# Optimization experiments

Hardware: AMD Instinct MI355X
Metric: run time of the kernel (lower is better)

Reference implementation:

```python
import jax, jax.numpy as jnp
import numpy as np

B, S, D, H = 8, 2048, 1024, 1024

def setup_inputs() -> dict:
    key = jax.random.key(0)
    ks = jax.random.split(key, 7)
    s = 1.0 / np.sqrt(D)  # torch Linear default init scale (uniform bound)
    x = jax.random.normal(ks[0], (B, S, D), dtype=jnp.float32)
    Wq = jax.random.uniform(ks[1], (D, H), jnp.float32, -s, s)
    bq = jax.random.uniform(ks[2], (H,), jnp.float32, -s, s)
    Wk = jax.random.uniform(ks[3], (D, H), jnp.float32, -s, s)
    bk = jax.random.uniform(ks[4], (H,), jnp.float32, -s, s)
    Wv = jax.random.uniform(ks[5], (D, H), jnp.float32, -s, s)
    bv = jax.random.uniform(ks[6], (H,), jnp.float32, -s, s)
    return {"x": x, "Wq": Wq, "bq": bq, "Wk": Wk, "bk": bk, "Wv": Wv, "bv": bv}

def reference(x, Wq, bq, Wk, bk, Wv, bv):
    scale = jnp.asarray(H ** 0.5, x.dtype)
    q = jnp.einsum('bsd,dh->bsh', x, Wq) + bq
    k = jnp.einsum('bsd,dh->bsh', x, Wk) + bk
    v = jnp.einsum('bsd,dh->bsh', x, Wv) + bv
    scores = jnp.einsum('bqh,bkh->bqk', q, k) / scale  # [B,S,S]
    probs = jax.nn.softmax(scores, axis=-1)
    return jnp.einsum('bqk,bkh->bqh', probs, v)
```

## Files before the change

kernel.cpp:

```cpp
#include <hip/hip_runtime.h>
#include <hip/hip_bf16.h>
#include <stdint.h>

using bf16 = __hip_bfloat16;
typedef __bf16 bf16x8 __attribute__((ext_vector_type(8)));
typedef float f32x4 __attribute__((ext_vector_type(4)));
typedef unsigned short u16x8 __attribute__((ext_vector_type(8)));

#define GLOAD_LDS16(gp, lp)                                                    \
  __builtin_amdgcn_global_load_lds(                                           \
      (const __attribute__((address_space(1))) void*)(gp),                     \
      (__attribute__((address_space(3))) void*)(lp), 16, 0, 0)

#define WAITCNT_VM(N) asm volatile("s_waitcnt vmcnt(" #N ")" ::: "memory")
#define SB0() __builtin_amdgcn_sched_barrier(0)

__device__ inline void store_out(bf16* p, float v)  { *p = __float2bfloat16(v); }
__device__ inline void store_out(float* p, float v) { *p = v; }

template <typename OUT_T, int BIAS_AXIS, bool NFAST>
__global__ __launch_bounds__(256, 2) void gemm_bm(
    const bf16* __restrict__ A, const bf16* __restrict__ Bt,
    const float* __restrict__ bias0, const float* __restrict__ bias1,
    OUT_T* __restrict__ out0, OUT_T* __restrict__ out1, int Nsplit,
    int K, int lda, int ldb, int ldc,
    long long sA, long long sB, long long sC, float alpha)
{
    __shared__ __align__(16) bf16 lds[36864];

    const int Mt = gridDim.x, Nt = gridDim.y;
    const int nwg = Mt * Nt * gridDim.z;
    const int hw  = blockIdx.x + Mt * (blockIdx.y + Nt * blockIdx.z);
    const int lg  = (nwg & 7) ? hw : ((hw & 7) * (nwg >> 3) + (hw >> 3));
    const int per = Mt * Nt;
    const int zt  = lg / per;
    const int rem = lg - zt * per;
    int mt, nt;
    if (NFAST) { mt = rem / Nt; nt = rem - mt * Nt; }
    else       { mt = rem % Mt; nt = rem / Mt; }

    A  += (long long)zt * sA;
    Bt += (long long)zt * sB;
    out0 += (long long)zt * sC;
    if (out1) out1 += (long long)zt * sC;

    const int bm = mt * 256;
    const int bn = nt * 128;
    const int t = threadIdx.x, lane = t & 63, w = t >> 6;
    const int wm = w >> 1, wn = w & 1;
    const int fr = lane & 15, c16 = lane >> 4;

    const bf16* gA[4];
    const bf16* gB[2];
    #pragma unroll
    for (int k = 0; k < 4; ++k) {
        const int idx = t + 256 * k, r = idx >> 2, c = idx & 3;
        gA[k] = A + (long long)(bm + r) * lda + ((c ^ ((r >> 1) & 3)) << 3);
    }
    #pragma unroll
    for (int k = 0; k < 2; ++k) {
        const int idx = t + 256 * k, r = idx >> 2, c = idx & 3;
        gB[k] = Bt + (long long)(bn + r) * ldb + ((c ^ ((r >> 1) & 3)) << 3);
    }
    const int dstA = t * 8;
    const int dstB = 8192 + t * 8;

#define STAGE(JT, SLOTB) do {                                                  \
    GLOAD_LDS16(gA[0] + (JT) * 32, &lds[(SLOTB) + dstA]);                      \
    GLOAD_LDS16(gA[1] + (JT) * 32, &lds[(SLOTB) + dstA + 2048]);               \
    GLOAD_LDS16(gA[2] + (JT) * 32, &lds[(SLOTB) + dstA + 4096]);               \
    GLOAD_LDS16(gA[3] + (JT) * 32, &lds[(SLOTB) + dstA + 6144]);               \
    GLOAD_LDS16(gB[0] + (JT) * 32, &lds[(SLOTB) + dstB]);                      \
    GLOAD_LDS16(gB[1] + (JT) * 32, &lds[(SLOTB) + dstB + 2048]);               \
} while (0)

    const int swz8 = (c16 ^ ((fr >> 1) & 3)) << 3;
    const int offA = (wm * 128 + fr) * 32 + swz8;
    const int offB = 8192 + (wn * 64 + fr) * 32 + swz8;

    const int nk = K >> 5;

    STAGE(0, 0); STAGE(1, 12288);
    WAITCNT_VM(6);
    __builtin_amdgcn_s_barrier();

    f32x4 acc[8][4] = {};

    int slotb = 0;
    for (int j = 0; j < nk; ++j) {
        SB0();

        bf16x8 af[8], bfv[4];
        #pragma unroll
        for (int m = 0; m < 8; ++m)
            af[m] = *reinterpret_cast<const bf16x8*>(&lds[slotb + offA + m * 512]);
        #pragma unroll
        for (int n = 0; n < 4; ++n)
            bfv[n] = *reinterpret_cast<const bf16x8*>(&lds[slotb + offB + n * 512]);

        if (j + 2 < nk) {
            int s2 = slotb + 24576; if (s2 >= 36864) s2 -= 36864;
            STAGE(j + 2, s2);
        }

        #pragma unroll
        for (int m = 0; m < 8; ++m)
            #pragma unroll
            for (int n = 0; n < 4; ++n)
                acc[m][n] = __builtin_amdgcn_mfma_f32_16x16x32_bf16(
                    af[m], bfv[n], acc[m][n], 0, 0, 0);

        SB0();
        if (j + 2 < nk)      { WAITCNT_VM(6); }
        else if (j + 1 < nk) { WAITCNT_VM(0); }
        __builtin_amdgcn_s_barrier();

        slotb += 12288; if (slotb == 36864) slotb = 0;
    }

    const int colbase = bn + wn * 64 + fr;
    const int rowbase = bm + wm * 128 + c16 * 4;
    #pragma unroll
    for (int n = 0; n < 4; ++n) {
        const int gc = colbase + n * 16;
        const bool seg0 = gc < Nsplit;
        OUT_T* op = seg0 ? out0 : out1;
        const int col = seg0 ? gc : gc - Nsplit;
        float bcol = 0.0f;
        if (BIAS_AXIS == 0) {
            const float* bp = seg0 ? bias0 : bias1;
            if (bp) bcol = bp[col];
        }
        #pragma unroll
        for (int m = 0; m < 8; ++m) {
            #pragma unroll
            for (int jj = 0; jj < 4; ++jj) {
                const int row = rowbase + m * 16 + jj;
                float v = acc[m][n][jj] * alpha;
                if (BIAS_AXIS == 0) v += bcol;
                else if (bias0)     v += bias0[row];
                store_out(&op[(long long)row * ldc + col], v);
            }
        }
    }
#undef STAGE
}

__global__ __launch_bounds__(256) void f32_to_bf16(
    const float* __restrict__ in, bf16* __restrict__ out, long long n)
{
    long long i = ((long long)blockIdx.x * 256 + threadIdx.x) * 4;
    const long long stride = (long long)gridDim.x * 256 * 4;
    for (; i < n; i += stride) {
        float4 v = *reinterpret_cast<const float4*>(in + i);
        unsigned ux = __float_as_uint(v.x), uy = __float_as_uint(v.y);
        unsigned uz = __float_as_uint(v.z), uw = __float_as_uint(v.w);
        ushort4 o;
        o.x = (unsigned short)((ux + 0x7fffu + ((ux >> 16) & 1u)) >> 16);
        o.y = (unsigned short)((uy + 0x7fffu + ((uy >> 16) & 1u)) >> 16);
        o.z = (unsigned short)((uz + 0x7fffu + ((uz >> 16) & 1u)) >> 16);
        o.w = (unsigned short)((uw + 0x7fffu + ((uw >> 16) & 1u)) >> 16);
        *reinterpret_cast<ushort4*>(out + i) = o;
    }
}

__global__ void transpose_f32_bf16(const float* __restrict__ in,
                                   bf16* __restrict__ out, int R, int C)
{
    __shared__ float tile[32][33];
    const int c0 = blockIdx.x * 32, r0 = blockIdx.y * 32;
    const int tx = threadIdx.x, ty = threadIdx.y;
    #pragma unroll
    for (int i = ty; i < 32; i += 8)
        tile[i][tx] = in[(long long)(r0 + i) * C + (c0 + tx)];
    __syncthreads();
    #pragma unroll
    for (int i = ty; i < 32; i += 8)
        out[(long long)(c0 + i) * R + (r0 + tx)] = __float2bfloat16(tile[tx][i]);
}

__global__ __launch_bounds__(256) void softmax_rows(bf16* __restrict__ Sbuf, int cols)
{
    __shared__ float red[8];
    bf16* p = Sbuf + (long long)blockIdx.x * cols;
    const int t = threadIdx.x;

    u16x8 v = *reinterpret_cast<const u16x8*>(p + t * 8);
    float f[8];
    #pragma unroll
    for (int i = 0; i < 8; ++i)
        f[i] = __uint_as_float((unsigned)v[i] << 16);

    float m = -3.0e38f;
    #pragma unroll
    for (int i = 0; i < 8; ++i) m = fmaxf(m, f[i]);
    #pragma unroll
    for (int o = 32; o; o >>= 1) m = fmaxf(m, __shfl_xor(m, o));
    if ((t & 63) == 0) red[t >> 6] = m;
    __syncthreads();
    m = fmaxf(fmaxf(red[0], red[1]), fmaxf(red[2], red[3]));

    float s = 0.0f;
    #pragma unroll
    for (int i = 0; i < 8; ++i) { f[i] = __expf(f[i] - m); s += f[i]; }
    #pragma unroll
    for (int o = 32; o; o >>= 1) s += __shfl_xor(s, o);
    __syncthreads();
    if ((t & 63) == 0) red[4 + (t >> 6)] = s;
    __syncthreads();
    s = (red[4] + red[5]) + (red[6] + red[7]);
    const float inv = 1.0f / s;

    u16x8 o16;
    #pragma unroll
    for (int i = 0; i < 8; ++i) {
        unsigned u = __float_as_uint(f[i] * inv);
        o16[i] = (unsigned short)((u + 0x7fffu + ((u >> 16) & 1u)) >> 16);
    }
    *reinterpret_cast<u16x8*>(p + t * 8) = o16;
}

extern "C" void kernel_launch(void* const* d_in, const int* in_sizes, int n_in,
                              void* d_out, int out_size, void* d_ws, size_t ws_size,
                              hipStream_t stream)
{
    const int B = 8, S = 2048, D = 1024, H = 1024;
    const float* x  = (const float*)d_in[0];
    const float* Wq = (const float*)d_in[1];
    const float* bq = (const float*)d_in[2];
    const float* Wk = (const float*)d_in[3];
    const float* bk = (const float*)d_in[4];
    const float* Wv = (const float*)d_in[5];
    const float* bv = (const float*)d_in[6];
    float* out = (float*)d_out;

    const size_t nQKV = (size_t)B * S * H;
    const size_t nW   = (size_t)D * H;
    const long long sSH = (long long)S * H;
    const long long sSS = (long long)S * S;

    dim3 tb(32, 8), g256(256);
    const float inv_scale = 1.0f / 32.0f;

    bf16* xb   = (bf16*)d_ws;
    bf16* Q    = xb  + nQKV;
    bf16* Kb   = Q   + nQKV;
    bf16* Vt   = Kb  + nQKV;
    bf16* WtQK = Vt  + nQKV;
    bf16* Wtv  = WtQK + 2 * nW;
    bf16* Sc   = Wtv + nW;

    const size_t tierA = (4 * nQKV + 3 * nW + (size_t)B * S * S) * 2;
    const size_t tierB = (4 * nQKV + 3 * nW + (size_t)S * S) * 2;
    const bool bigA = ws_size >= tierA;
    if (ws_size < tierB) return;

    f32_to_bf16<<<dim3(2048), g256, 0, stream>>>(x, xb, (long long)nQKV);
    transpose_f32_bf16<<<dim3(H / 32, D / 32), tb, 0, stream>>>(Wq, WtQK, D, H);
    transpose_f32_bf16<<<dim3(H / 32, D / 32), tb, 0, stream>>>(Wk, WtQK + nW, D, H);
    transpose_f32_bf16<<<dim3(H / 32, D / 32), tb, 0, stream>>>(Wv, Wtv, D, H);

    gemm_bm<bf16, 0, true><<<dim3(B * S / 256, 2 * H / 128, 1), g256, 0, stream>>>(
        xb, WtQK, bq, bk, Q, Kb, H, D, D, D, H, 0, 0, 0, 1.0f);

    gemm_bm<bf16, 1, false><<<dim3(H / 256, B * S / 128, 1), g256, 0, stream>>>(
        Wtv, xb, bv, nullptr, Vt, nullptr, 1 << 30, D, D, D, B * S, 0, 0, 0, 1.0f);

    if (bigA) {
        gemm_bm<bf16, 0, true><<<dim3(S / 256, S / 128, B), g256, 0, stream>>>(
            Q, Kb, nullptr, nullptr, Sc, nullptr, 1 << 30, H, H, H, S,
            sSH, sSH, sSS, inv_scale);
        softmax_rows<<<dim3(B * S), g256, 0, stream>>>(Sc, S);
        gemm_bm<float, 0, true><<<dim3(S / 256, H / 128, B), g256, 0, stream>>>(
            Sc, Vt, nullptr, nullptr, out, nullptr, 1 << 30, S, S, B * S, H,
            sSS, (long long)S, sSH, 1.0f);
    } else {
        for (int b = 0; b < B; ++b) {
            gemm_bm<bf16, 0, true><<<dim3(S / 256, S / 128, 1), g256, 0, stream>>>(
                Q + (size_t)b * sSH, Kb + (size_t)b * sSH, nullptr, nullptr,
                Sc, nullptr, 1 << 30, H, H, H, S, 0, 0, 0, inv_scale);
            softmax_rows<<<dim3(S), g256, 0, stream>>>(Sc, S);
            gemm_bm<float, 0, true><<<dim3(S / 256, H / 128, 1), g256, 0, stream>>>(
                Sc, Vt + (size_t)b * S, nullptr, nullptr,
                out + (size_t)b * sSH, nullptr, 1 << 30, S, S, B * S, H,
                0, 0, 0, 1.0f);
        }
    }
}
```

Baseline: 330.6 us.

## Load GEMM B fragments directly from global into registers, drop NFAST ordering

The B operand tile no longer goes through LDS. Each wave loads its four B fragments straight from global memory into double-buffered registers one k-step ahead, and only the A tile stays staged in the triple-buffered LDS ring, which shrinks LDS use. The NFAST tile ordering is removed, so all launches now walk M-tiles fastest. The aim is to cut LDS traffic and footprint, at the cost of redundant global reads of B across the waves that share it and a changed L2 locality pattern for the launches that used N-fast ordering.

Measured after the change: 440.8 us. +33.3%, slower.

```diff
diff --git a/kernel.cpp b/kernel.cpp
--- a/kernel.cpp
+++ b/kernel.cpp
@@ -18,7 +18,7 @@
 __device__ inline void store_out(bf16* p, float v)  { *p = __float2bfloat16(v); }
 __device__ inline void store_out(float* p, float v) { *p = v; }
 
-template <typename OUT_T, int BIAS_AXIS, bool NFAST>
+template <typename OUT_T, int BIAS_AXIS>
 __global__ __launch_bounds__(256, 2) void gemm_bm(
     const bf16* __restrict__ A, const bf16* __restrict__ Bt,
     const float* __restrict__ bias0, const float* __restrict__ bias1,
@@ -26,7 +26,7 @@
     int K, int lda, int ldb, int ldc,
     long long sA, long long sB, long long sC, float alpha)
 {
-    __shared__ __align__(16) bf16 lds[36864];
+    __shared__ __align__(16) bf16 lds[24576];
 
     const int Mt = gridDim.x, Nt = gridDim.y;
     const int nwg = Mt * Nt * gridDim.z;
@@ -35,9 +35,8 @@
     const int per = Mt * Nt;
     const int zt  = lg / per;
     const int rem = lg - zt * per;
-    int mt, nt;
-    if (NFAST) { mt = rem / Nt; nt = rem - mt * Nt; }
-    else       { mt = rem % Mt; nt = rem / Mt; }
+    const int mt  = rem % Mt;
+    const int nt  = rem / Mt;
 
     A  += (long long)zt * sA;
     Bt += (long long)zt * sB;
@@ -51,72 +50,73 @@
     const int fr = lane & 15, c16 = lane >> 4;
 
     const bf16* gA[4];
-    const bf16* gB[2];
     #pragma unroll
     for (int k = 0; k < 4; ++k) {
         const int idx = t + 256 * k, r = idx >> 2, c = idx & 3;
         gA[k] = A + (long long)(bm + r) * lda + ((c ^ ((r >> 1) & 3)) << 3);
     }
-    #pragma unroll
-    for (int k = 0; k < 2; ++k) {
-        const int idx = t + 256 * k, r = idx >> 2, c = idx & 3;
-        gB[k] = Bt + (long long)(bn + r) * ldb + ((c ^ ((r >> 1) & 3)) << 3);
-    }
     const int dstA = t * 8;
-    const int dstB = 8192 + t * 8;
 
 #define STAGE(JT, SLOTB) do {                                                  \
     GLOAD_LDS16(gA[0] + (JT) * 32, &lds[(SLOTB) + dstA]);                      \
     GLOAD_LDS16(gA[1] + (JT) * 32, &lds[(SLOTB) + dstA + 2048]);               \
     GLOAD_LDS16(gA[2] + (JT) * 32, &lds[(SLOTB) + dstA + 4096]);               \
     GLOAD_LDS16(gA[3] + (JT) * 32, &lds[(SLOTB) + dstA + 6144]);               \
-    GLOAD_LDS16(gB[0] + (JT) * 32, &lds[(SLOTB) + dstB]);                      \
-    GLOAD_LDS16(gB[1] + (JT) * 32, &lds[(SLOTB) + dstB + 2048]);               \
+} while (0)
+
+    const bf16* pBf[4];
+    #pragma unroll
+    for (int nf = 0; nf < 4; ++nf)
+        pBf[nf] = Bt + (long long)(bn + wn * 64 + nf * 16 + fr) * ldb + c16 * 8;
+
+#define BLOAD(JT, DST) do {                                                    \
+    _Pragma("unroll") for (int nf = 0; nf < 4; ++nf)                           \
+        DST[nf] = *reinterpret_cast<const bf16x8*>(pBf[nf] + (JT) * 32);       \
 } while (0)
 
     const int swz8 = (c16 ^ ((fr >> 1) & 3)) << 3;
     const int offA = (wm * 128 + fr) * 32 + swz8;
-    const int offB = 8192 + (wn * 64 + fr) * 32 + swz8;
 
     const int nk = K >> 5;
 
-    STAGE(0, 0); STAGE(1, 12288);
-    WAITCNT_VM(6);
+    f32x4 acc[8][4] = {};
+    bf16x8 bU[4], bV[4];
+
+    STAGE(0, 0);
+    BLOAD(0, bU);
+    STAGE(1, 8192);
+    WAITCNT_VM(4);
     __builtin_amdgcn_s_barrier();
 
-    f32x4 acc[8][4] = {};
+#define STEP(J, SLOTB, BCUR, BNXT) do {                                        \
+    SB0();                                                                     \
+    bf16x8 af[8];                                                              \
+    _Pragma("unroll") for (int m = 0; m < 8; ++m)                              \
+        af[m] = *reinterpret_cast<const bf16x8*>(&lds[(SLOTB) + offA + m*512]);\
+    if ((J) + 1 < nk) BLOAD((J) + 1, BNXT);                                    \
+    if ((J) + 2 < nk) {                                                        \
+        int s2 = (SLOTB) + 16384; if (s2 >= 24576) s2 -= 24576;                \
+        STAGE((J) + 2, s2);                                                    \
+    }                                                                          \
+    _Pragma("unroll") for (int m = 0; m < 8; ++m)                              \
+        _Pragma("unroll") for (int n = 0; n < 4; ++n)                          \
+            acc[m][n] = __builtin_amdgcn_mfma_f32_16x16x32_bf16(               \
+                af[m], BCUR[n], acc[m][n], 0, 0, 0);                           \
+    SB0();                                                                     \
+    if ((J) + 2 < nk)      { WAITCNT_VM(4); __builtin_amdgcn_s_barrier(); }    \
+    else if ((J) + 1 < nk) { WAITCNT_VM(0); __builtin_amdgcn_s_barrier(); }    \
+} while (0)
 
     int slotb = 0;
-    for (int j = 0; j < nk; ++j) {
-        SB0();
-
-        bf16x8 af[8], bfv[4];
-        #pragma unroll
-        for (int m = 0; m < 8; ++m)
-            af[m] = *reinterpret_cast<const bf16x8*>(&lds[slotb + offA + m * 512]);
-        #pragma unroll
-        for (int n = 0; n < 4; ++n)
-            bfv[n] = *reinterpret_cast<const bf16x8*>(&lds[slotb + offB + n * 512]);
-
-        if (j + 2 < nk) {
-            int s2 = slotb + 24576; if (s2 >= 36864) s2 -= 36864;
-            STAGE(j + 2, s2);
-        }
-
-        #pragma unroll
-        for (int m = 0; m < 8; ++m)
-            #pragma unroll
-            for (int n = 0; n < 4; ++n)
-                acc[m][n] = __builtin_amdgcn_mfma_f32_16x16x32_bf16(
-                    af[m], bfv[n], acc[m][n], 0, 0, 0);
-
-        SB0();
-        if (j + 2 < nk)      { WAITCNT_VM(6); }
-        else if (j + 1 < nk) { WAITCNT_VM(0); }
-        __builtin_amdgcn_s_barrier();
-
-        slotb += 12288; if (slotb == 36864) slotb = 0;
-    }
+    for (int j = 0; j < nk; j += 2) {
+        STEP(j, slotb, bU, bV);
+        slotb += 8192; if (slotb == 24576) slotb = 0;
+        STEP(j + 1, slotb, bV, bU);
+        slotb += 8192; if (slotb == 24576) slotb = 0;
+    }
+#undef STEP
+#undef STAGE
+#undef BLOAD
 
     const int colbase = bn + wn * 64 + fr;
     const int rowbase = bm + wm * 128 + c16 * 4;
@@ -143,7 +143,6 @@
             }
         }
     }
-#undef STAGE
 }
 
 __global__ __launch_bounds__(256) void f32_to_bf16(
@@ -260,27 +259,27 @@
     transpose_f32_bf16<<<dim3(H / 32, D / 32), tb, 0, stream>>>(Wk, WtQK + nW, D, H);
     transpose_f32_bf16<<<dim3(H / 32, D / 32), tb, 0, stream>>>(Wv, Wtv, D, H);
 
-    gemm_bm<bf16, 0, true><<<dim3(B * S / 256, 2 * H / 128, 1), g256, 0, stream>>>(
+    gemm_bm<bf16, 0><<<dim3(B * S / 256, 2 * H / 128, 1), g256, 0, stream>>>(
         xb, WtQK, bq, bk, Q, Kb, H, D, D, D, H, 0, 0, 0, 1.0f);
 
-    gemm_bm<bf16, 1, false><<<dim3(H / 256, B * S / 128, 1), g256, 0, stream>>>(
+    gemm_bm<bf16, 1><<<dim3(H / 256, B * S / 128, 1), g256, 0, stream>>>(
         Wtv, xb, bv, nullptr, Vt, nullptr, 1 << 30, D, D, D, B * S, 0, 0, 0, 1.0f);
 
     if (bigA) {
-        gemm_bm<bf16, 0, true><<<dim3(S / 256, S / 128, B), g256, 0, stream>>>(
+        gemm_bm<bf16, 0><<<dim3(S / 256, S / 128, B), g256, 0, stream>>>(
             Q, Kb, nullptr, nullptr, Sc, nullptr, 1 << 30, H, H, H, S,
             sSH, sSH, sSS, inv_scale);
         softmax_rows<<<dim3(B * S), g256, 0, stream>>>(Sc, S);
-        gemm_bm<float, 0, true><<<dim3(S / 256, H / 128, B), g256, 0, stream>>>(
+        gemm_bm<float, 0><<<dim3(S / 256, H / 128, B), g256, 0, stream>>>(
             Sc, Vt, nullptr, nullptr, out, nullptr, 1 << 30, S, S, B * S, H,
             sSS, (long long)S, sSH, 1.0f);
     } else {
         for (int b = 0; b < B; ++b) {
-            gemm_bm<bf16, 0, true><<<dim3(S / 256, S / 128, 1), g256, 0, stream>>>(
+            gemm_bm<bf16, 0><<<dim3(S / 256, S / 128, 1), g256, 0, stream>>>(
                 Q + (size_t)b * sSH, Kb + (size_t)b * sSH, nullptr, nullptr,
                 Sc, nullptr, 1 << 30, H, H, H, S, 0, 0, 0, inv_scale);
             softmax_rows<<<dim3(S), g256, 0, stream>>>(Sc, S);
-            gemm_bm<float, 0, true><<<dim3(S / 256, H / 128, 1), g256, 0, stream>>>(
+            gemm_bm<float, 0><<<dim3(S / 256, H / 128, 1), g256, 0, stream>>>(
                 Sc, Vt + (size_t)b * S, nullptr, nullptr,
                 out + (size_t)b * sSH, nullptr, 1 << 30, S, S, B * S, H,
                 0, 0, 0, 1.0f);
```
